# Kernel optimization log

Measured on AMD Instinct MI355X. Metric: run time of the kernel, lower is better.

Reference implementation:

```python
import jax, jax.numpy as jnp
import numpy as np

B, S, D = 2, 2048, 1024
H = 16
HS = D // H  # head_size = 64
SCALE = HS ** 0.5


def setup_inputs() -> dict:
    key = jax.random.key(0)
    ks = jax.random.split(key, 7)
    std = 1.0 / np.sqrt(D)
    return {
        "x": jax.random.normal(ks[0], (B, S, D), dtype=jnp.float32),
        "Wq": jax.random.normal(ks[1], (D, D), dtype=jnp.float32) * std,
        "bq": jax.random.normal(ks[2], (D,), dtype=jnp.float32) * std,
        "Wk": jax.random.normal(ks[3], (D, D), dtype=jnp.float32) * std,
        "bk": jax.random.normal(ks[4], (D,), dtype=jnp.float32) * std,
        "Wv": jax.random.normal(ks[5], (D, D), dtype=jnp.float32) * std,
        "bv": jax.random.normal(ks[6], (D,), dtype=jnp.float32) * std,
    }


def reference(x, Wq, bq, Wk, bk, Wv, bv):
    bs, seq, _ = x.shape
    # QKV projections (torch Linear: x @ W.T + b)
    Q = (x @ Wq.T + bq).reshape(bs, seq, H, HS)
    K = (x @ Wk.T + bk).reshape(bs, seq, H, HS)
    V = (x @ Wv.T + bv).reshape(bs, seq, H, HS)
    # scores[b,h,q,k] = Q . K / scale
    scores = jnp.einsum("bqhd,bkhd->bhqk", Q, K) / SCALE
    # causal mask: disallow k > q
    causal = jnp.triu(jnp.ones((seq, seq), dtype=bool), k=1)
    scores = jnp.where(causal, -jnp.inf, scores)
    probs = jax.nn.softmax(scores, axis=-1)
    att = jnp.einsum("bhqk,bkhd->bqhd", probs, V)
    return att.reshape(bs, seq, H * HS)
```

## Files before the change

### kernel.cpp

```cpp
#include <hip/hip_runtime.h>

typedef unsigned short ushort_t;
typedef __bf16 bf16x8 __attribute__((ext_vector_type(8)));
typedef unsigned short ushortx8 __attribute__((ext_vector_type(8)));
typedef unsigned short ushortx4 __attribute__((ext_vector_type(4)));
typedef unsigned int uintx4 __attribute__((ext_vector_type(4)));
typedef float floatx4 __attribute__((ext_vector_type(4)));
typedef float floatx16 __attribute__((ext_vector_type(16)));

__device__ inline void load16_lds(const ushort_t* g, ushort_t* l) {
  __builtin_amdgcn_global_load_lds(
      (__attribute__((address_space(1))) void*)(g),
      (__attribute__((address_space(3))) void*)(l),
      16, 0, 0);
}

__device__ inline float bf2f(ushort_t u) {
  unsigned int v = ((unsigned int)u) << 16;
  return __builtin_bit_cast(float, v);
}

__device__ inline ushort_t f2bf(float f) {
  unsigned int u = __builtin_bit_cast(unsigned int, f);
  u += 0x7fffu + ((u >> 16) & 1u);
  return (ushort_t)(u >> 16);
}

__device__ inline bf16x8 ldfrag(const ushort_t* p) {
  return __builtin_bit_cast(bf16x8, *(const ushortx8*)p);
}

__device__ inline unsigned cvtpk_bf16(float lo, float hi) {
  unsigned r;
  asm("v_cvt_pk_bf16_f32 %0, %1, %2" : "=v"(r) : "v"(lo), "v"(hi));
  return r;
}

__device__ inline void plswap(unsigned& a, unsigned& b) {
  asm("v_permlane32_swap_b32 %0, %1" : "+v"(a), "+v"(b));
}

__device__ inline bool sniff_f32(const ushort_t* x, int lane_off) {
  float v = fabsf(bf2f(x[lane_off]));
  bool big = !(v < 1e4f);
  return __ballot(big) != 0ull;
}

__global__ __launch_bounds__(256) void convert_all(
    const void* __restrict__ x,
    const void* __restrict__ wq, const void* __restrict__ wk, const void* __restrict__ wv,
    const void* __restrict__ bq, const void* __restrict__ bk, const void* __restrict__ bv,
    ushort_t* __restrict__ xb, ushort_t* __restrict__ wqb,
    ushort_t* __restrict__ wkb, ushort_t* __restrict__ wvb,
    float* __restrict__ biasf, int* __restrict__ flag)
{
  const bool f32 = sniff_f32((const ushort_t*)x, (int)(threadIdx.x & 63));
  const int seg = blockIdx.y;
  if (seg == 4) {
    if (blockIdx.x == 0 && threadIdx.x == 0) *flag = f32 ? 1 : 0;
    const int i = blockIdx.x * 256 + threadIdx.x;
    if (i >= 1024) return;
    const void* bs[3] = {bq, bk, bv};
#pragma unroll
    for (int k = 0; k < 3; ++k)
      biasf[k * 1024 + i] = f32 ? ((const float*)bs[k])[i] : bf2f(((const ushort_t*)bs[k])[i]);
    return;
  }
  const void* src = (seg == 0) ? x : (seg == 1) ? wq : (seg == 2) ? wk : wv;
  ushort_t* dst   = (seg == 0) ? xb : (seg == 1) ? wqb : (seg == 2) ? wkb : wvb;
  const int n = (seg == 0) ? 4194304 : 1048576;
  const int i = (blockIdx.x * 256 + threadIdx.x) * 8;
  if (i >= n) return;
  if (f32) {
    const float* s = (const float*)src + i;
    ushortx8 o;
#pragma unroll
    for (int j = 0; j < 8; ++j) o[j] = f2bf(s[j]);
    *(ushortx8*)(dst + i) = o;
  } else {
    *(ushortx8*)(dst + i) = *(const ushortx8*)((const ushort_t*)src + i);
  }
}

__global__ __launch_bounds__(256, 2) void qkv_gemm(
    const ushort_t* __restrict__ x,
    const ushort_t* __restrict__ Wq, const ushort_t* __restrict__ Wk,
    const ushort_t* __restrict__ Wv, const float* __restrict__ biasf,
    ushort_t* __restrict__ Qo, ushort_t* __restrict__ Ko, ushort_t* __restrict__ Vt)
{
  __shared__ __attribute__((aligned(16))) ushort_t As[128 * 32];
  __shared__ __attribute__((aligned(16))) ushort_t Bs[128 * 32];

  const int which = blockIdx.z;
  const ushort_t* W = (which == 0) ? Wq : (which == 1) ? Wk : Wv;
  const float oscale = (which == 0) ? 0.18033688011112042f : 1.0f;

  const int n0 = blockIdx.x * 128;
  const int m0 = blockIdx.y * 128;

  const int tid  = threadIdx.x;
  const int wave = tid >> 6;
  const int lane = tid & 63;
  const int ln   = lane & 15;
  const int quad = lane >> 4;
  const int wm = (wave >> 1) * 64;
  const int wn = (wave & 1) * 64;

  floatx4 acc[4][4];
#pragma unroll
  for (int i = 0; i < 4; ++i)
#pragma unroll
    for (int j = 0; j < 4; ++j) acc[i][j] = floatx4{0.f, 0.f, 0.f, 0.f};

  const int c1 = tid, c2 = tid + 256;
  const ushort_t* ga1 = x + (m0 + (c1 >> 2)) * 1024 + (c1 & 3) * 8;
  const ushort_t* ga2 = x + (m0 + (c2 >> 2)) * 1024 + (c2 & 3) * 8;
  const ushort_t* gb1 = W + (n0 + (c1 >> 2)) * 1024 + (c1 & 3) * 8;
  const ushort_t* gb2 = W + (n0 + (c2 >> 2)) * 1024 + (c2 & 3) * 8;
  ushort_t* la1 = As + wave * 512;
  ushort_t* la2 = As + 2048 + wave * 512;
  ushort_t* lb1 = Bs + wave * 512;
  ushort_t* lb2 = Bs + 2048 + wave * 512;

  for (int kt = 0; kt < 1024; kt += 32) {
    __syncthreads();
    load16_lds(ga1 + kt, la1);
    load16_lds(ga2 + kt, la2);
    load16_lds(gb1 + kt, lb1);
    load16_lds(gb2 + kt, lb2);
    __syncthreads();

    bf16x8 af[4], bfr[4];
#pragma unroll
    for (int mi = 0; mi < 4; ++mi)
      af[mi] = ldfrag(As + (wm + mi * 16 + ln) * 32 + quad * 8);
#pragma unroll
    for (int ni = 0; ni < 4; ++ni)
      bfr[ni] = ldfrag(Bs + (wn + ni * 16 + ln) * 32 + quad * 8);
#pragma unroll
    for (int mi = 0; mi < 4; ++mi)
#pragma unroll
      for (int ni = 0; ni < 4; ++ni)
        acc[mi][ni] = __builtin_amdgcn_mfma_f32_16x16x32_bf16(af[mi], bfr[ni], acc[mi][ni], 0, 0, 0);
  }

  float bvv[4];
#pragma unroll
  for (int ni = 0; ni < 4; ++ni) bvv[ni] = biasf[which * 1024 + n0 + wn + ni * 16 + ln];

  if (which == 2) {
#pragma unroll
    for (int mi = 0; mi < 4; ++mi)
#pragma unroll
      for (int ni = 0; ni < 4; ++ni) {
        const int col = n0 + wn + ni * 16 + ln;
        const int row0 = m0 + wm + mi * 16 + quad * 4;
        const int b = row0 >> 11, s0 = row0 & 2047;
        const int h = col >> 6, hs = col & 63;
        ushortx4 pk;
#pragma unroll
        for (int r = 0; r < 4; ++r) pk[r] = f2bf(acc[mi][ni][r] + bvv[ni]);
        *(ushortx4*)(Vt + ((size_t)((b * 16 + h) * 64 + hs)) * 2048 + s0) = pk;
      }
  } else {
    ushort_t* out = (which == 0) ? Qo : Ko;
#pragma unroll
    for (int mi = 0; mi < 4; ++mi)
#pragma unroll
      for (int ni = 0; ni < 4; ++ni) {
        const int col = n0 + wn + ni * 16 + ln;
#pragma unroll
        for (int r = 0; r < 4; ++r) {
          const int row = m0 + wm + mi * 16 + quad * 4 + r;
          out[row * 1024 + col] = f2bf((acc[mi][ni][r] + bvv[ni]) * oscale);
        }
      }
  }
}

__global__ __launch_bounds__(128) void flash14(
    const ushort_t* __restrict__ Q, const ushort_t* __restrict__ Kx,
    const ushort_t* __restrict__ Vt, void* __restrict__ out,
    const int* __restrict__ flag)
{
  __shared__ __attribute__((aligned(16))) float Cb[64][68];
  __shared__ float lbufW[64];
  __shared__ float ILi[64];

  const bool f32o = (*flag != 0);
  const int tid  = threadIdx.x;
  const int wave = tid >> 6;
  const int lane = tid & 63;
  const int l31 = lane & 31;
  const int hi  = lane >> 5;

#define CROW(r) (((r) & 3) + 8 * ((r) >> 2) + 4 * hi)

  const int i = blockIdx.x;
  const int xcd = i & 7, j = i >> 3;
  const int bh = xcd * 4 + (j & 3);
  const int cc = 31 - (j >> 2);
  const int b = bh >> 4, h = bh & 15;
  const int qw = cc * 64;
  const int ntiles = cc + 1;

  const ushort_t* kbase = Kx + ((size_t)b * 2048) * 1024 + h * 64;
  const ushort_t* vbase = Vt + (size_t)bh * 64 * 2048;

  bf16x8 qf[2][4];
#pragma unroll
  for (int qq = 0; qq < 2; ++qq)
#pragma unroll
    for (int s = 0; s < 4; ++s)
      qf[qq][s] = ldfrag(Q + (size_t)(b * 2048 + qw + 32 * qq + l31) * 1024 + h * 64 + s * 16 + hi * 8);

  floatx16 ot[2][2];
#pragma unroll
  for (int qq = 0; qq < 2; ++qq)
#pragma unroll
    for (int dq = 0; dq < 2; ++dq)
#pragma unroll
      for (int r = 0; r < 16; ++r) ot[qq][dq][r] = 0.f;
  float li[2] = {0.f, 0.f};

  bf16x8 kfA[8], kfB[8], vf[8];

#define LOADK(KF, KV0) do {                                                   \
    const ushort_t* kp_ = kbase + (size_t)((KV0) + l31) * 1024 + hi * 8;      \
    KF[0] = ldfrag(kp_);       KF[1] = ldfrag(kp_ + 16);                      \
    KF[2] = ldfrag(kp_ + 32);  KF[3] = ldfrag(kp_ + 48);                      \
    const ushort_t* kq_ = kp_ + 32 * 1024;                                    \
    KF[4] = ldfrag(kq_);       KF[5] = ldfrag(kq_ + 16);                      \
    KF[6] = ldfrag(kq_ + 32);  KF[7] = ldfrag(kq_ + 48);                      \
  } while (0)

#define LOADV(KV0) do {                                                       \
    const ushort_t* vp0_ = vbase + (size_t)l31 * 2048 + (KV0) + hi * 8;       \
    vf[0] = ldfrag(vp0_);       vf[1] = ldfrag(vp0_ + 16);                    \
    vf[2] = ldfrag(vp0_ + 32);  vf[3] = ldfrag(vp0_ + 48);                    \
    const ushort_t* vp1_ = vp0_ + (size_t)32 * 2048;                          \
    vf[4] = ldfrag(vp1_);       vf[5] = ldfrag(vp1_ + 16);                    \
    vf[6] = ldfrag(vp1_ + 32);  vf[7] = ldfrag(vp1_ + 48);                    \
  } while (0)

#define PACK_PV(PARR, SH, SIDX, QQ) do {                                      \
    unsigned X_ = cvtpk_bf16(PARR[8 * (SH) + 0], PARR[8 * (SH) + 1]);         \
    unsigned Y_ = cvtpk_bf16(PARR[8 * (SH) + 2], PARR[8 * (SH) + 3]);         \
    unsigned Z_ = cvtpk_bf16(PARR[8 * (SH) + 4], PARR[8 * (SH) + 5]);         \
    unsigned W_ = cvtpk_bf16(PARR[8 * (SH) + 6], PARR[8 * (SH) + 7]);         \
    plswap(X_, Z_);                                                           \
    plswap(Y_, W_);                                                           \
    uintx4 u_ = {X_, Y_, Z_, W_};                                             \
    const bf16x8 pa_ = __builtin_bit_cast(bf16x8, u_);                        \
    ot[QQ][0] = __builtin_amdgcn_mfma_f32_32x32x16_bf16(pa_, vf[(SIDX)], ot[QQ][0], 0, 0, 0);     \
    ot[QQ][1] = __builtin_amdgcn_mfma_f32_32x32x16_bf16(pa_, vf[4 + (SIDX)], ot[QQ][1], 0, 0, 0); \
  } while (0)

#define SHALF(KF, KOFF, KVADD, SIDX0, SIDX1, QQ) do {                         \
    floatx16 st_;                                                             \
    _Pragma("unroll")                                                         \
    for (int r = 0; r < 16; ++r) st_[r] = 0.f;                                \
    _Pragma("unroll")                                                         \
    for (int s = 0; s < 4; ++s)                                               \
      st_ = __builtin_amdgcn_mfma_f32_32x32x16_bf16(KF[(KOFF) + s], qf[QQ][s], st_, 0, 0, 0); \
    float p_[16];                                                             \
    if (diag_) {                                                              \
      const int qg_ = qw + 32 * (QQ) + l31;                                   \
      _Pragma("unroll")                                                       \
      for (int r = 0; r < 16; ++r) {                                          \
        const int kva_ = kv0_ + (KVADD) + CROW(r);                            \
        const float e_ = __builtin_amdgcn_exp2f(st_[r]);                      \
        p_[r] = (kva_ > qg_) ? 0.f : e_;                                      \
      }                                                                       \
    } else {                                                                  \
      _Pragma("unroll")                                                       \
      for (int r = 0; r < 16; ++r) p_[r] = __builtin_amdgcn_exp2f(st_[r]);    \
    }                                                                         \
    float ls_ = 0.f;                                                          \
    _Pragma("unroll")                                                         \
    for (int r = 0; r < 16; ++r) ls_ += p_[r];                                \
    li[QQ] += ls_;                                                            \
    PACK_PV(p_, 0, SIDX0, QQ);                                                \
    PACK_PV(p_, 1, SIDX1, QQ);                                                \
  } while (0)

#define TILE32(KF, T) do {                                                    \
    const int kv0_ = (T) * 64;                                                \
    const bool diag_ = ((T) == ntiles - 1);                                   \
    _Pragma("unroll")                                                         \
    for (int qq = 0; qq < 2; ++qq) {                                          \
      SHALF(KF, 0, 0, 0, 1, qq);                                              \
      SHALF(KF, 4, 32, 2, 3, qq);                                             \
    }                                                                         \
  } while (0)

  int t = wave;
  if (t < ntiles) LOADK(kfA, t * 64);
  for (; t < ntiles; t += 4) {
    LOADV(t * 64);
    if (t + 2 < ntiles) LOADK(kfB, (t + 2) * 64);
    TILE32(kfA, t);
    if (t + 2 < ntiles) {
      LOADV((t + 2) * 64);
      if (t + 4 < ntiles) LOADK(kfA, (t + 4) * 64);
      TILE32(kfB, t + 2);
    }
  }

#undef LOADK
#undef LOADV
#undef PACK_PV
#undef SHALF
#undef TILE32

  float lf[2];
#pragma unroll
  for (int qq = 0; qq < 2; ++qq) lf[qq] = li[qq] + __shfl_xor(li[qq], 32);

  if (wave == 1) {
#pragma unroll
    for (int qq = 0; qq < 2; ++qq) {
#pragma unroll
      for (int dq = 0; dq < 2; ++dq)
#pragma unroll
        for (int r = 0; r < 16; ++r)
          Cb[32 * qq + CROW(r)][32 * dq + l31] = ot[qq][dq][r];
      lbufW[32 * qq + l31] = lf[qq];
    }
  }
  __syncthreads();
  if (wave == 0) {
#pragma unroll
    for (int qq = 0; qq < 2; ++qq) {
#pragma unroll
      for (int dq = 0; dq < 2; ++dq)
#pragma unroll
        for (int r = 0; r < 16; ++r)
          ot[qq][dq][r] += Cb[32 * qq + CROW(r)][32 * dq + l31];
      lf[qq] += lbufW[32 * qq + l31];
      ILi[32 * qq + l31] = 1.0f / lf[qq];
    }

#pragma unroll
    for (int qq = 0; qq < 2; ++qq) {
#pragma unroll
      for (int r = 0; r < 16; ++r) {
        const int q_ = qw + 32 * qq + CROW(r);
        const float iv = ILi[32 * qq + CROW(r)];
        if (f32o) {
          float* of = (float*)out;
#pragma unroll
          for (int dq = 0; dq < 2; ++dq)
            of[(size_t)(b * 2048 + q_) * 1024 + h * 64 + 32 * dq + l31] = ot[qq][dq][r] * iv;
        } else {
          ushort_t* ob = (ushort_t*)out;
#pragma unroll
          for (int dq = 0; dq < 2; ++dq)
            ob[(size_t)(b * 2048 + q_) * 1024 + h * 64 + 32 * dq + l31] = f2bf(ot[qq][dq][r] * iv);
        }
      }
    }
  }
#undef CROW
}

extern "C" void kernel_launch(void* const* d_in, const int* in_sizes, int n_in,
                              void* d_out, int out_size, void* d_ws, size_t ws_size,
                              hipStream_t stream) {
  char* w = (char*)d_ws;
  int* flag = (int*)w;
  size_t off = 256;
  ushort_t* xb  = (ushort_t*)(w + off); off += (size_t)4194304 * 2;
  ushort_t* wqb = (ushort_t*)(w + off); off += (size_t)1048576 * 2;
  ushort_t* wkb = (ushort_t*)(w + off); off += (size_t)1048576 * 2;
  ushort_t* wvb = (ushort_t*)(w + off); off += (size_t)1048576 * 2;
  float* biasf  = (float*)(w + off);    off += (size_t)3 * 1024 * 4;
  ushort_t* Qw  = (ushort_t*)(w + off); off += (size_t)4194304 * 2;
  ushort_t* Kw  = (ushort_t*)(w + off); off += (size_t)4194304 * 2;
  ushort_t* Vtw = (ushort_t*)(w + off);

  convert_all<<<dim3(2048, 5), 256, 0, stream>>>(
      d_in[0], d_in[1], d_in[3], d_in[5], d_in[2], d_in[4], d_in[6],
      xb, wqb, wkb, wvb, biasf, flag);
  qkv_gemm<<<dim3(8, 32, 3), 256, 0, stream>>>(xb, wqb, wkb, wvb, biasf, Qw, Kw, Vtw);
  flash14<<<1024, 128, 0, stream>>>(Qw, Kw, Vtw, d_out, flag);
}
```

Before: 161.2 us.

## Halve flash attention query tile to 32 rows and double grid

Each attention block now handles 32 query rows instead of 64, and the grid doubles to 2048 blocks. This lowers per-block register use and gives finer-grained load balance across CUs for the causal triangle. On the diagonal tile, the second 32-key half is skipped when it is fully masked. In exchange, each K/V tile loaded from memory is reused by half as many query rows, so global/L2 traffic per FLOP rises.

Result: slower. 185.8 us (+15.2%).

```diff
diff --git a/kernel.cpp b/kernel.cpp
--- a/kernel.cpp
+++ b/kernel.cpp
@@ -178,14 +178,14 @@
   }
 }
 
-__global__ __launch_bounds__(128) void flash14(
+__global__ __launch_bounds__(128) void flash15(
     const ushort_t* __restrict__ Q, const ushort_t* __restrict__ Kx,
     const ushort_t* __restrict__ Vt, void* __restrict__ out,
     const int* __restrict__ flag)
 {
-  __shared__ __attribute__((aligned(16))) float Cb[64][68];
-  __shared__ float lbufW[64];
-  __shared__ float ILi[64];
+  __shared__ __attribute__((aligned(16))) float Cb[32][68];
+  __shared__ float lbufW[32];
+  __shared__ float ILi[32];
 
   const bool f32o = (*flag != 0);
   const int tid  = threadIdx.x;
@@ -199,29 +199,25 @@
   const int i = blockIdx.x;
   const int xcd = i & 7, j = i >> 3;
   const int bh = xcd * 4 + (j & 3);
-  const int cc = 31 - (j >> 2);
+  const int cc = 63 - (j >> 2);
   const int b = bh >> 4, h = bh & 15;
-  const int qw = cc * 64;
-  const int ntiles = cc + 1;
+  const int qw = cc * 32;
+  const int ntiles = (cc >> 1) + 1;
 
   const ushort_t* kbase = Kx + ((size_t)b * 2048) * 1024 + h * 64;
   const ushort_t* vbase = Vt + (size_t)bh * 64 * 2048;
 
-  bf16x8 qf[2][4];
-#pragma unroll
-  for (int qq = 0; qq < 2; ++qq)
-#pragma unroll
-    for (int s = 0; s < 4; ++s)
-      qf[qq][s] = ldfrag(Q + (size_t)(b * 2048 + qw + 32 * qq + l31) * 1024 + h * 64 + s * 16 + hi * 8);
-
-  floatx16 ot[2][2];
-#pragma unroll
-  for (int qq = 0; qq < 2; ++qq)
-#pragma unroll
-    for (int dq = 0; dq < 2; ++dq)
-#pragma unroll
-      for (int r = 0; r < 16; ++r) ot[qq][dq][r] = 0.f;
-  float li[2] = {0.f, 0.f};
+  bf16x8 qf[4];
+#pragma unroll
+  for (int s = 0; s < 4; ++s)
+    qf[s] = ldfrag(Q + (size_t)(b * 2048 + qw + l31) * 1024 + h * 64 + s * 16 + hi * 8);
+
+  floatx16 ot[2];
+#pragma unroll
+  for (int dq = 0; dq < 2; ++dq)
+#pragma unroll
+    for (int r = 0; r < 16; ++r) ot[dq][r] = 0.f;
+  float li = 0.f;
 
   bf16x8 kfA[8], kfB[8], vf[8];
 
@@ -243,7 +239,7 @@
     vf[6] = ldfrag(vp1_ + 32);  vf[7] = ldfrag(vp1_ + 48);                    \
   } while (0)
 
-#define PACK_PV(PARR, SH, SIDX, QQ) do {                                      \
+#define PACK_PV(PARR, SH, SIDX) do {                                          \
     unsigned X_ = cvtpk_bf16(PARR[8 * (SH) + 0], PARR[8 * (SH) + 1]);         \
     unsigned Y_ = cvtpk_bf16(PARR[8 * (SH) + 2], PARR[8 * (SH) + 3]);         \
     unsigned Z_ = cvtpk_bf16(PARR[8 * (SH) + 4], PARR[8 * (SH) + 5]);         \
@@ -252,20 +248,20 @@
     plswap(Y_, W_);                                                           \
     uintx4 u_ = {X_, Y_, Z_, W_};                                             \
     const bf16x8 pa_ = __builtin_bit_cast(bf16x8, u_);                        \
-    ot[QQ][0] = __builtin_amdgcn_mfma_f32_32x32x16_bf16(pa_, vf[(SIDX)], ot[QQ][0], 0, 0, 0);     \
-    ot[QQ][1] = __builtin_amdgcn_mfma_f32_32x32x16_bf16(pa_, vf[4 + (SIDX)], ot[QQ][1], 0, 0, 0); \
-  } while (0)
-
-#define SHALF(KF, KOFF, KVADD, SIDX0, SIDX1, QQ) do {                         \
+    ot[0] = __builtin_amdgcn_mfma_f32_32x32x16_bf16(pa_, vf[(SIDX)], ot[0], 0, 0, 0);     \
+    ot[1] = __builtin_amdgcn_mfma_f32_32x32x16_bf16(pa_, vf[4 + (SIDX)], ot[1], 0, 0, 0); \
+  } while (0)
+
+#define SHALF(KF, KOFF, KVADD, SIDX0, SIDX1) do {                             \
     floatx16 st_;                                                             \
     _Pragma("unroll")                                                         \
     for (int r = 0; r < 16; ++r) st_[r] = 0.f;                                \
     _Pragma("unroll")                                                         \
     for (int s = 0; s < 4; ++s)                                               \
-      st_ = __builtin_amdgcn_mfma_f32_32x32x16_bf16(KF[(KOFF) + s], qf[QQ][s], st_, 0, 0, 0); \
+      st_ = __builtin_amdgcn_mfma_f32_32x32x16_bf16(KF[(KOFF) + s], qf[s], st_, 0, 0, 0); \
     float p_[16];                                                             \
     if (diag_) {                                                              \
-      const int qg_ = qw + 32 * (QQ) + l31;                                   \
+      const int qg_ = qw + l31;                                               \
       _Pragma("unroll")                                                       \
       for (int r = 0; r < 16; ++r) {                                          \
         const int kva_ = kv0_ + (KVADD) + CROW(r);                            \
@@ -279,19 +275,16 @@
     float ls_ = 0.f;                                                          \
     _Pragma("unroll")                                                         \
     for (int r = 0; r < 16; ++r) ls_ += p_[r];                                \
-    li[QQ] += ls_;                                                            \
-    PACK_PV(p_, 0, SIDX0, QQ);                                                \
-    PACK_PV(p_, 1, SIDX1, QQ);                                                \
+    li += ls_;                                                                \
+    PACK_PV(p_, 0, SIDX0);                                                    \
+    PACK_PV(p_, 1, SIDX1);                                                    \
   } while (0)
 
 #define TILE32(KF, T) do {                                                    \
     const int kv0_ = (T) * 64;                                                \
     const bool diag_ = ((T) == ntiles - 1);                                   \
-    _Pragma("unroll")                                                         \
-    for (int qq = 0; qq < 2; ++qq) {                                          \
-      SHALF(KF, 0, 0, 0, 1, qq);                                              \
-      SHALF(KF, 4, 32, 2, 3, qq);                                             \
-    }                                                                         \
+    SHALF(KF, 0, 0, 0, 1);                                                    \
+    if (!(diag_ && (kv0_ + 32 > qw + 31))) SHALF(KF, 4, 32, 2, 3);            \
   } while (0)
 
   int t = wave;
@@ -313,51 +306,40 @@
 #undef SHALF
 #undef TILE32
 
-  float lf[2];
-#pragma unroll
-  for (int qq = 0; qq < 2; ++qq) lf[qq] = li[qq] + __shfl_xor(li[qq], 32);
+  float lf = li + __shfl_xor(li, 32);
 
   if (wave == 1) {
 #pragma unroll
-    for (int qq = 0; qq < 2; ++qq) {
-#pragma unroll
-      for (int dq = 0; dq < 2; ++dq)
-#pragma unroll
-        for (int r = 0; r < 16; ++r)
-          Cb[32 * qq + CROW(r)][32 * dq + l31] = ot[qq][dq][r];
-      lbufW[32 * qq + l31] = lf[qq];
-    }
+    for (int dq = 0; dq < 2; ++dq)
+#pragma unroll
+      for (int r = 0; r < 16; ++r)
+        Cb[CROW(r)][32 * dq + l31] = ot[dq][r];
+    lbufW[l31] = lf;
   }
   __syncthreads();
   if (wave == 0) {
 #pragma unroll
-    for (int qq = 0; qq < 2; ++qq) {
-#pragma unroll
-      for (int dq = 0; dq < 2; ++dq)
-#pragma unroll
-        for (int r = 0; r < 16; ++r)
-          ot[qq][dq][r] += Cb[32 * qq + CROW(r)][32 * dq + l31];
-      lf[qq] += lbufW[32 * qq + l31];
-      ILi[32 * qq + l31] = 1.0f / lf[qq];
-    }
-
-#pragma unroll
-    for (int qq = 0; qq < 2; ++qq) {
-#pragma unroll
-      for (int r = 0; r < 16; ++r) {
-        const int q_ = qw + 32 * qq + CROW(r);
-        const float iv = ILi[32 * qq + CROW(r)];
-        if (f32o) {
-          float* of = (float*)out;
-#pragma unroll
-          for (int dq = 0; dq < 2; ++dq)
-            of[(size_t)(b * 2048 + q_) * 1024 + h * 64 + 32 * dq + l31] = ot[qq][dq][r] * iv;
-        } else {
-          ushort_t* ob = (ushort_t*)out;
-#pragma unroll
-          for (int dq = 0; dq < 2; ++dq)
-            ob[(size_t)(b * 2048 + q_) * 1024 + h * 64 + 32 * dq + l31] = f2bf(ot[qq][dq][r] * iv);
-        }
+    for (int dq = 0; dq < 2; ++dq)
+#pragma unroll
+      for (int r = 0; r < 16; ++r)
+        ot[dq][r] += Cb[CROW(r)][32 * dq + l31];
+    lf += lbufW[l31];
+    ILi[l31] = 1.0f / lf;
+
+#pragma unroll
+    for (int r = 0; r < 16; ++r) {
+      const int q_ = qw + CROW(r);
+      const float iv = ILi[CROW(r)];
+      if (f32o) {
+        float* of = (float*)out;
+#pragma unroll
+        for (int dq = 0; dq < 2; ++dq)
+          of[(size_t)(b * 2048 + q_) * 1024 + h * 64 + 32 * dq + l31] = ot[dq][r] * iv;
+      } else {
+        ushort_t* ob = (ushort_t*)out;
+#pragma unroll
+        for (int dq = 0; dq < 2; ++dq)
+          ob[(size_t)(b * 2048 + q_) * 1024 + h * 64 + 32 * dq + l31] = f2bf(ot[dq][r] * iv);
       }
     }
   }
@@ -383,5 +365,5 @@
       d_in[0], d_in[1], d_in[3], d_in[5], d_in[2], d_in[4], d_in[6],
       xb, wqb, wkb, wvb, biasf, flag);
   qkv_gemm<<<dim3(8, 32, 3), 256, 0, stream>>>(xb, wqb, wkb, wvb, biasf, Qw, Kw, Vtw);
-  flash14<<<1024, 128, 0, stream>>>(Qw, Kw, Vtw, d_out, flag);
-}
+  flash15<<<2048, 128, 0, stream>>>(Qw, Kw, Vtw, d_out, flag);
+}
```

## Double-buffer V fragments, add MFMA priority hints, skip fully-masked diagonal half

Applied to the files above, without the earlier changes.

V fragments now get their own double buffer and are prefetched one tile ahead together with K, so V loads are no longer issued just before use. MFMA blocks are wrapped in s_setprio raises to favour matrix issue over other waves. On the diagonal tile, the second key half for the first query half is skipped because it is entirely masked. These changes add register pressure from the extra eight V fragment registers, which may reduce occupancy.

Measured after the change: 161.1 us. About the same (-0.1%).

```diff
diff --git a/kernel.cpp b/kernel.cpp
--- a/kernel.cpp
+++ b/kernel.cpp
@@ -178,7 +178,7 @@
   }
 }
 
-__global__ __launch_bounds__(128) void flash14(
+__global__ __launch_bounds__(128) void flash17(
     const ushort_t* __restrict__ Q, const ushort_t* __restrict__ Kx,
     const ushort_t* __restrict__ Vt, void* __restrict__ out,
     const int* __restrict__ flag)
@@ -223,7 +223,7 @@
       for (int r = 0; r < 16; ++r) ot[qq][dq][r] = 0.f;
   float li[2] = {0.f, 0.f};
 
-  bf16x8 kfA[8], kfB[8], vf[8];
+  bf16x8 kfA[8], kfB[8], vfA[8], vfB[8];
 
 #define LOADK(KF, KV0) do {                                                   \
     const ushort_t* kp_ = kbase + (size_t)((KV0) + l31) * 1024 + hi * 8;      \
@@ -234,16 +234,16 @@
     KF[6] = ldfrag(kq_ + 32);  KF[7] = ldfrag(kq_ + 48);                      \
   } while (0)
 
-#define LOADV(KV0) do {                                                       \
+#define LOADV(VF, KV0) do {                                                   \
     const ushort_t* vp0_ = vbase + (size_t)l31 * 2048 + (KV0) + hi * 8;       \
-    vf[0] = ldfrag(vp0_);       vf[1] = ldfrag(vp0_ + 16);                    \
-    vf[2] = ldfrag(vp0_ + 32);  vf[3] = ldfrag(vp0_ + 48);                    \
+    VF[0] = ldfrag(vp0_);       VF[1] = ldfrag(vp0_ + 16);                    \
+    VF[2] = ldfrag(vp0_ + 32);  VF[3] = ldfrag(vp0_ + 48);                    \
     const ushort_t* vp1_ = vp0_ + (size_t)32 * 2048;                          \
-    vf[4] = ldfrag(vp1_);       vf[5] = ldfrag(vp1_ + 16);                    \
-    vf[6] = ldfrag(vp1_ + 32);  vf[7] = ldfrag(vp1_ + 48);                    \
-  } while (0)
-
-#define PACK_PV(PARR, SH, SIDX, QQ) do {                                      \
+    VF[4] = ldfrag(vp1_);       VF[5] = ldfrag(vp1_ + 16);                    \
+    VF[6] = ldfrag(vp1_ + 32);  VF[7] = ldfrag(vp1_ + 48);                    \
+  } while (0)
+
+#define PACK_PV(VF, PARR, SH, SIDX, QQ) do {                                  \
     unsigned X_ = cvtpk_bf16(PARR[8 * (SH) + 0], PARR[8 * (SH) + 1]);         \
     unsigned Y_ = cvtpk_bf16(PARR[8 * (SH) + 2], PARR[8 * (SH) + 3]);         \
     unsigned Z_ = cvtpk_bf16(PARR[8 * (SH) + 4], PARR[8 * (SH) + 5]);         \
@@ -252,17 +252,21 @@
     plswap(Y_, W_);                                                           \
     uintx4 u_ = {X_, Y_, Z_, W_};                                             \
     const bf16x8 pa_ = __builtin_bit_cast(bf16x8, u_);                        \
-    ot[QQ][0] = __builtin_amdgcn_mfma_f32_32x32x16_bf16(pa_, vf[(SIDX)], ot[QQ][0], 0, 0, 0);     \
-    ot[QQ][1] = __builtin_amdgcn_mfma_f32_32x32x16_bf16(pa_, vf[4 + (SIDX)], ot[QQ][1], 0, 0, 0); \
-  } while (0)
-
-#define SHALF(KF, KOFF, KVADD, SIDX0, SIDX1, QQ) do {                         \
+    __builtin_amdgcn_s_setprio(1);                                            \
+    ot[QQ][0] = __builtin_amdgcn_mfma_f32_32x32x16_bf16(pa_, VF[(SIDX)], ot[QQ][0], 0, 0, 0);     \
+    ot[QQ][1] = __builtin_amdgcn_mfma_f32_32x32x16_bf16(pa_, VF[4 + (SIDX)], ot[QQ][1], 0, 0, 0); \
+    __builtin_amdgcn_s_setprio(0);                                            \
+  } while (0)
+
+#define SHALF(KF, VF, KOFF, KVADD, SIDX0, SIDX1, QQ) do {                     \
     floatx16 st_;                                                             \
     _Pragma("unroll")                                                         \
     for (int r = 0; r < 16; ++r) st_[r] = 0.f;                                \
+    __builtin_amdgcn_s_setprio(1);                                            \
     _Pragma("unroll")                                                         \
     for (int s = 0; s < 4; ++s)                                               \
       st_ = __builtin_amdgcn_mfma_f32_32x32x16_bf16(KF[(KOFF) + s], qf[QQ][s], st_, 0, 0, 0); \
+    __builtin_amdgcn_s_setprio(0);                                            \
     float p_[16];                                                             \
     if (diag_) {                                                              \
       const int qg_ = qw + 32 * (QQ) + l31;                                   \
@@ -280,30 +284,27 @@
     _Pragma("unroll")                                                         \
     for (int r = 0; r < 16; ++r) ls_ += p_[r];                                \
     li[QQ] += ls_;                                                            \
-    PACK_PV(p_, 0, SIDX0, QQ);                                                \
-    PACK_PV(p_, 1, SIDX1, QQ);                                                \
-  } while (0)
-
-#define TILE32(KF, T) do {                                                    \
+    PACK_PV(VF, p_, 0, SIDX0, QQ);                                            \
+    PACK_PV(VF, p_, 1, SIDX1, QQ);                                            \
+  } while (0)
+
+#define TILE32(KF, VF, T) do {                                                \
     const int kv0_ = (T) * 64;                                                \
     const bool diag_ = ((T) == ntiles - 1);                                   \
-    _Pragma("unroll")                                                         \
-    for (int qq = 0; qq < 2; ++qq) {                                          \
-      SHALF(KF, 0, 0, 0, 1, qq);                                              \
-      SHALF(KF, 4, 32, 2, 3, qq);                                             \
-    }                                                                         \
+    SHALF(KF, VF, 0, 0, 0, 1, 0);                                             \
+    if (!diag_) SHALF(KF, VF, 4, 32, 2, 3, 0);                                \
+    SHALF(KF, VF, 0, 0, 0, 1, 1);                                             \
+    SHALF(KF, VF, 4, 32, 2, 3, 1);                                            \
   } while (0)
 
   int t = wave;
-  if (t < ntiles) LOADK(kfA, t * 64);
+  if (t < ntiles) { LOADK(kfA, t * 64); LOADV(vfA, t * 64); }
   for (; t < ntiles; t += 4) {
-    LOADV(t * 64);
-    if (t + 2 < ntiles) LOADK(kfB, (t + 2) * 64);
-    TILE32(kfA, t);
+    if (t + 2 < ntiles) { LOADK(kfB, (t + 2) * 64); LOADV(vfB, (t + 2) * 64); }
+    TILE32(kfA, vfA, t);
     if (t + 2 < ntiles) {
-      LOADV((t + 2) * 64);
-      if (t + 4 < ntiles) LOADK(kfA, (t + 4) * 64);
-      TILE32(kfB, t + 2);
+      if (t + 4 < ntiles) { LOADK(kfA, (t + 4) * 64); LOADV(vfA, (t + 4) * 64); }
+      TILE32(kfB, vfB, t + 2);
     }
   }
 
@@ -383,5 +384,5 @@
       d_in[0], d_in[1], d_in[3], d_in[5], d_in[2], d_in[4], d_in[6],
       xb, wqb, wkb, wvb, biasf, flag);
   qkv_gemm<<<dim3(8, 32, 3), 256, 0, stream>>>(xb, wqb, wkb, wvb, biasf, Qw, Kw, Vtw);
-  flash14<<<1024, 128, 0, stream>>>(Qw, Kw, Vtw, d_out, flag);
-}
+  flash17<<<1024, 128, 0, stream>>>(Qw, Kw, Vtw, d_out, flag);
+}
```
